# Kernel tuning notes

Hardware: AMD Instinct MI355X
Metric: run time of the kernel (lower is better)

The kernel has to match this reference:

```python
import jax, jax.numpy as jnp
import numpy as np

TRIPLET_MARGIN = 0.2
ATN_ALPHA = 0.1
ATN_BETA = 1.05
ATN_WEIGHT = 1.0
EPS = 1e-8


def _normalize(x):
    return x / jnp.maximum(jnp.linalg.norm(x, axis=-1, keepdims=True), EPS)


def _cos_dist_rowwise(a, b):  # [N,d],[N,d] -> [N]
    return 1.0 - jnp.sum(_normalize(a) * _normalize(b), axis=-1)


def _cos_dist_matrix(a, b):  # [N,d],[C,d] -> [N,C]
    return 1.0 - _normalize(a) @ _normalize(b).T


def setup_inputs() -> dict:
    key = jax.random.key(0)
    ks = jax.random.split(key, 5)
    N, D, C = 65536, 512, 16
    return {
        "anchor": jax.random.normal(ks[0], (N, D), jnp.float32),
        "positive": jax.random.normal(ks[1], (N, D), jnp.float32),
        "negative": jax.random.normal(ks[2], (N, D), jnp.float32),
        "embeddings": jax.random.normal(ks[3], (N, D), jnp.float32),
        "labels": jax.random.randint(ks[4], (N,), 0, C, jnp.int32),
        "num_classes": C,
    }


def reference(anchor, positive, negative, embeddings, labels, num_classes):
    # --- Triplet loss ---
    pos_dist = _cos_dist_rowwise(anchor, positive)
    neg_dist = _cos_dist_rowwise(anchor, negative)
    triplet = jnp.mean(jax.nn.relu(pos_dist - neg_dist + TRIPLET_MARGIN))

    # --- Augmented Triplet (ATN) loss ---
    N = embeddings.shape[0]
    counts = jax.ops.segment_sum(jnp.ones((N,), embeddings.dtype), labels,
                                 num_segments=num_classes)  # [C]
    sums = jax.ops.segment_sum(embeddings, labels, num_segments=num_classes)  # [C,d]
    centroids = sums / jnp.maximum(counts, 1.0)[:, None]
    present = counts > 0  # [C]

    cdist = _cos_dist_matrix(centroids, centroids)  # [C,C]
    eye = jnp.eye(num_classes, dtype=bool)
    pair = (cdist <= ATN_BETA) & ~eye & present[:, None] & present[None, :]  # symmetric
    pair_f = pair.astype(embeddings.dtype)
    cnt = pair_f.sum(axis=1)  # close pairs per class [C]

    D = _cos_dist_matrix(embeddings, centroids)  # [N,C]
    d_own = jnp.take_along_axis(D, labels[:, None], axis=1)[:, 0]  # [N]
    w = cnt[labels]  # multiplicity of each sample in intra/inter terms [N]

    intra_sum = jnp.sum(w * jax.nn.relu(d_own - ATN_ALPHA))
    inter_sum = jnp.sum(pair_f[labels] * jax.nn.relu(ATN_BETA - D))
    n_terms = jnp.sum(w)  # identical count for intra and inter lists
    safe_n = jnp.maximum(n_terms, 1.0)
    atn = jnp.where(n_terms > 0, intra_sum / safe_n + inter_sum / safe_n, 0.0)

    return triplet + ATN_WEIGHT * atn
```

## Files before the change

### kernel.cpp

```cpp
#include <hip/hip_runtime.h>

#define EPSN   1e-8f
#define MARGIN 0.2f
#define ALPHA  0.1f
#define BETA   1.05f
#define DIM    512
#define NCLS   16
#define NSTR   516

typedef __attribute__((ext_vector_type(8))) short short8;
typedef __attribute__((ext_vector_type(4))) float f32x4;
typedef __attribute__((ext_vector_type(4))) float nf4;

__device__ __forceinline__ unsigned short f2bf(float f) {
    unsigned u = __float_as_uint(f);
    return (unsigned short)((u + 0x7FFFu + ((u >> 16) & 1u)) >> 16);
}
__device__ __forceinline__ short8 pack8(float4 x0, float4 x1) {
    short8 r;
    r[0] = (short)f2bf(x0.x); r[1] = (short)f2bf(x0.y);
    r[2] = (short)f2bf(x0.z); r[3] = (short)f2bf(x0.w);
    r[4] = (short)f2bf(x1.x); r[5] = (short)f2bf(x1.y);
    r[6] = (short)f2bf(x1.z); r[7] = (short)f2bf(x1.w);
    return r;
}


__global__ __launch_bounds__(256) void k_init(const int* __restrict__ L,
                                              float* __restrict__ wsw,
                                              int* __restrict__ cpart, int N) {
    __shared__ int hist[NCLS];
    int t = threadIdx.x, bid = blockIdx.x;
    int gid = bid * 256 + t;
    for (int i = gid; i < 8192; i += 64 * 256) wsw[i] = 0.f;
    if (t < NCLS) hist[t] = 0;
    __syncthreads();
    int chunk = N >> 6;
    int base = bid * chunk;
    for (int i = t * 4; i < chunk; i += 1024) {
        int4 l4 = *(const int4*)(L + base + i);
        atomicAdd(&hist[l4.x], 1);
        atomicAdd(&hist[l4.y], 1);
        atomicAdd(&hist[l4.z], 1);
        atomicAdd(&hist[l4.w], 1);
    }
    __syncthreads();
    if (t < NCLS) cpart[bid * NCLS + t] = hist[t];
}

__global__ __launch_bounds__(256) void k_triplet(const float* __restrict__ A,
                                                 const float* __restrict__ P,
                                                 const float* __restrict__ Q,
                                                 float* __restrict__ tripart, int N) {
    __shared__ float red[4];
    int t = threadIdx.x, lane = t & 63, wid = t >> 6;
    int g = lane >> 4, seg = lane & 15;
    int gw = blockIdx.x * 4 + wid, nw = gridDim.x * 4;
    int nquad = N >> 2;
    float tri = 0.f;
    for (int quad = gw; quad < nquad; quad += 2 * nw) {
        int quadB = quad + nw;
        bool hasB = quadB < nquad;
        size_t base0 = (size_t)(quad * 4 + g) * DIM + seg * 4;
        size_t base1 = hasB ? ((size_t)(quadB * 4 + g) * DIM + seg * 4) : base0;
        nf4 a0[8], p0[8], q0[8], a1[8], p1[8], q1[8];
#pragma unroll
        for (int i = 0; i < 8; ++i) a0[i] = __builtin_nontemporal_load((const nf4*)(A + base0 + i * 64));
#pragma unroll
        for (int i = 0; i < 8; ++i) p0[i] = __builtin_nontemporal_load((const nf4*)(P + base0 + i * 64));
#pragma unroll
        for (int i = 0; i < 8; ++i) q0[i] = __builtin_nontemporal_load((const nf4*)(Q + base0 + i * 64));
#pragma unroll
        for (int i = 0; i < 8; ++i) a1[i] = __builtin_nontemporal_load((const nf4*)(A + base1 + i * 64));
#pragma unroll
        for (int i = 0; i < 8; ++i) p1[i] = __builtin_nontemporal_load((const nf4*)(P + base1 + i * 64));
#pragma unroll
        for (int i = 0; i < 8; ++i) q1[i] = __builtin_nontemporal_load((const nf4*)(Q + base1 + i * 64));
        {
            float sa = 0, sp = 0, sn = 0, dap = 0, dan = 0;
#pragma unroll
            for (int i = 0; i < 8; ++i) {
                sa  = fmaf(a0[i].x,a0[i].x, fmaf(a0[i].y,a0[i].y, fmaf(a0[i].z,a0[i].z, fmaf(a0[i].w,a0[i].w, sa))));
                sp  = fmaf(p0[i].x,p0[i].x, fmaf(p0[i].y,p0[i].y, fmaf(p0[i].z,p0[i].z, fmaf(p0[i].w,p0[i].w, sp))));
                sn  = fmaf(q0[i].x,q0[i].x, fmaf(q0[i].y,q0[i].y, fmaf(q0[i].z,q0[i].z, fmaf(q0[i].w,q0[i].w, sn))));
                dap = fmaf(a0[i].x,p0[i].x, fmaf(a0[i].y,p0[i].y, fmaf(a0[i].z,p0[i].z, fmaf(a0[i].w,p0[i].w, dap))));
                dan = fmaf(a0[i].x,q0[i].x, fmaf(a0[i].y,q0[i].y, fmaf(a0[i].z,q0[i].z, fmaf(a0[i].w,q0[i].w, dan))));
            }
#pragma unroll
            for (int o = 1; o < 16; o <<= 1) {
                sa  += __shfl_xor(sa,  o);
                sp  += __shfl_xor(sp,  o);
                sn  += __shfl_xor(sn,  o);
                dap += __shfl_xor(dap, o);
                dan += __shfl_xor(dan, o);
            }
            if (seg == 0) {
                float na = fmaxf(sqrtf(sa), EPSN);
                float np = fmaxf(sqrtf(sp), EPSN);
                float nn = fmaxf(sqrtf(sn), EPSN);
                tri += fmaxf((1.f - dap / (na * np)) - (1.f - dan / (na * nn)) + MARGIN, 0.f);
            }
        }
        if (hasB) {
            float sa = 0, sp = 0, sn = 0, dap = 0, dan = 0;
#pragma unroll
            for (int i = 0; i < 8; ++i) {
                sa  = fmaf(a1[i].x,a1[i].x, fmaf(a1[i].y,a1[i].y, fmaf(a1[i].z,a1[i].z, fmaf(a1[i].w,a1[i].w, sa))));
                sp  = fmaf(p1[i].x,p1[i].x, fmaf(p1[i].y,p1[i].y, fmaf(p1[i].z,p1[i].z, fmaf(p1[i].w,p1[i].w, sp))));
                sn  = fmaf(q1[i].x,q1[i].x, fmaf(q1[i].y,q1[i].y, fmaf(q1[i].z,q1[i].z, fmaf(q1[i].w,q1[i].w, sn))));
                dap = fmaf(a1[i].x,p1[i].x, fmaf(a1[i].y,p1[i].y, fmaf(a1[i].z,p1[i].z, fmaf(a1[i].w,p1[i].w, dap))));
                dan = fmaf(a1[i].x,q1[i].x, fmaf(a1[i].y,q1[i].y, fmaf(a1[i].z,q1[i].z, fmaf(a1[i].w,q1[i].w, dan))));
            }
#pragma unroll
            for (int o = 1; o < 16; o <<= 1) {
                sa  += __shfl_xor(sa,  o);
                sp  += __shfl_xor(sp,  o);
                sn  += __shfl_xor(sn,  o);
                dap += __shfl_xor(dap, o);
                dan += __shfl_xor(dan, o);
            }
            if (seg == 0) {
                float na = fmaxf(sqrtf(sa), EPSN);
                float np = fmaxf(sqrtf(sp), EPSN);
                float nn = fmaxf(sqrtf(sn), EPSN);
                tri += fmaxf((1.f - dap / (na * np)) - (1.f - dan / (na * nn)) + MARGIN, 0.f);
            }
        }
    }
    tri += __shfl_xor(tri, 16);
    tri += __shfl_xor(tri, 32);
    if (lane == 0) red[wid] = tri;
    __syncthreads();
    if (t == 0) tripart[blockIdx.x] = red[0] + red[1] + red[2] + red[3];
}

__global__ __launch_bounds__(256) void k_segsum(const float* __restrict__ E,
                                                const int* __restrict__ L,
                                                float* __restrict__ sums, int N) {
    __shared__ float acc[NCLS * 256];
    int t = threadIdx.x;
    int half = blockIdx.x & 1;
    int rg = blockIdx.x >> 1;
    int rpg = N >> 9;
    int r0 = rg * rpg;
    for (int i = t; i < NCLS * 256; i += 256) acc[i] = 0.f;
    __syncthreads();
    const float* Eh = E + half * 256 + t;
    for (int r = r0; r < r0 + rpg; r += 16) {
        int l[16];
        float v[16];
#pragma unroll
        for (int i = 0; i < 16; ++i) l[i] = L[r + i];
#pragma unroll
        for (int i = 0; i < 16; ++i) v[i] = Eh[(size_t)(r + i) * DIM];
#pragma unroll
        for (int i = 0; i < 16; ++i) acc[l[i] * 256 + t] += v[i];
    }
    __syncthreads();
#pragma unroll
    for (int c = 0; c < NCLS; ++c)
        atomicAdd(&sums[c * DIM + half * 256 + t], acc[c * 256 + t]);
}

__global__ __launch_bounds__(256) void k_centroid(const int* __restrict__ cpart,
                                                  const float* __restrict__ sums,
                                                  unsigned short* __restrict__ ncnh,
                                                  float* __restrict__ pr_g,
                                                  float* __restrict__ cf_g,
                                                  float* __restrict__ ntv) {
    __shared__ float ncns[NCLS * NSTR];
    __shared__ float prs[NCLS * NCLS];
    __shared__ float cntl[NCLS];
    int t = threadIdx.x;
    if (t < NCLS) {
        int s = 0;
        for (int b = 0; b < 64; ++b) s += cpart[b * NCLS + t];
        cntl[t] = (float)s;
    }
    __syncthreads();
    {
        int c = t >> 4, sI = t & 15;
        float inv = 1.f / fmaxf(cntl[c], 1.f);
        float4 v[8];
        float ssq = 0.f;
#pragma unroll
        for (int i = 0; i < 8; ++i) {
            v[i] = *(const float4*)(sums + c * DIM + sI * 32 + i * 4);
            v[i].x *= inv; v[i].y *= inv; v[i].z *= inv; v[i].w *= inv;
            ssq = fmaf(v[i].x, v[i].x, fmaf(v[i].y, v[i].y, fmaf(v[i].z, v[i].z, fmaf(v[i].w, v[i].w, ssq))));
        }
#pragma unroll
        for (int o = 1; o < 16; o <<= 1) ssq += __shfl_xor(ssq, o);
        float rs = 1.f / fmaxf(sqrtf(ssq), EPSN);
#pragma unroll
        for (int i = 0; i < 8; ++i) {
            float4 w = v[i];
            w.x *= rs; w.y *= rs; w.z *= rs; w.w *= rs;
            *(float4*)&ncns[c * NSTR + sI * 32 + i * 4] = w;
            ushort4 h;
            h.x = f2bf(w.x); h.y = f2bf(w.y); h.z = f2bf(w.z); h.w = f2bf(w.w);
            *(ushort4*)(ncnh + c * DIM + sI * 32 + i * 4) = h;
        }
    }
    __syncthreads();
    {
        int i = t >> 4, j = t & 15;
        float dot = 0.f;
        for (int d = 0; d < DIM; d += 4) {
            float4 a = *(const float4*)&ncns[i * NSTR + d];
            float4 b = *(const float4*)&ncns[j * NSTR + d];
            dot = fmaf(a.x, b.x, fmaf(a.y, b.y, fmaf(a.z, b.z, fmaf(a.w, b.w, dot))));
        }
        float cd = 1.f - dot;
        float pf = (cd <= BETA && i != j && cntl[i] > 0.f && cntl[j] > 0.f) ? 1.f : 0.f;
        prs[t] = pf;
        pr_g[t] = pf;
    }
    __syncthreads();
    if (t < NCLS) {
        float s = 0.f;
#pragma unroll
        for (int k = 0; k < NCLS; ++k) s += prs[t * 16 + k];
        cf_g[t] = s;
        cntl[t] = cntl[t] * s;
    }
    __syncthreads();
    if (t == 0) {
        float nt = 0.f;
#pragma unroll
        for (int k = 0; k < NCLS; ++k) nt += cntl[k];
        ntv[0] = nt;
        ntv[1] = 1.f / fmaxf(nt, 1.f);
    }
}

__global__ __launch_bounds__(256) void k_atn(const float* __restrict__ E,
                                             const int* __restrict__ L,
                                             const unsigned short* __restrict__ ncnh,
                                             const float* __restrict__ pr_g,
                                             const float* __restrict__ cf_g,
                                             float* __restrict__ atnpart,
                                             int nblk, int N) {
    __shared__ short bsh[16 * 4 * 16 * 8];
    __shared__ float pr[NCLS * NCLS];
    __shared__ float cf[NCLS];
    __shared__ float red[8];
    int t = threadIdx.x, lane = t & 63, wid = t >> 6;
    pr[t] = pr_g[t];
    if (t < NCLS) cf[t] = cf_g[t];
    {
        int ccol = t & 15, ckg = (t >> 4) & 3, sb = t >> 6;
#pragma unroll
        for (int i = 0; i < 4; ++i) {
            int s = sb * 4 + i;
            uint4 w = *(const uint4*)(ncnh + ccol * DIM + s * 32 + ckg * 8);
            *(uint4*)&bsh[((s * 4 + ckg) * 16 + ccol) * 8] = w;
        }
    }
    __syncthreads();

    int col = lane & 15;
    int kg = lane >> 4;
    const short* bbase = &bsh[(kg * 16 + col) * 8];

    float inter = 0.f, intra = 0.f;
    int gw = blockIdx.x * 4 + wid, nw = gridDim.x * 4;
    int ntile = N >> 4;
    for (int tile = gw; tile < ntile; tile += nw) {
        int rowb = tile << 4;
        int lval = L[rowb + col];
        const float* ar = E + (size_t)(rowb + col) * DIM + kg * 8;
        f32x4 ac0 = {0,0,0,0}, ac1 = {0,0,0,0}, ac2 = {0,0,0,0}, ac3 = {0,0,0,0};
        float ss0 = 0.f, ss1 = 0.f, ss2 = 0.f, ss3 = 0.f;
#pragma unroll
        for (int sg = 0; sg < 4; ++sg) {
            float4 x[8];
#pragma unroll
            for (int k = 0; k < 8; ++k)
                x[k] = *(const float4*)(ar + sg * 128 + (k >> 1) * 32 + (k & 1) * 4);
            {
                float4 u = x[0], v = x[1];
                short8 bf = *(const short8*)(bbase + (sg * 4 + 0) * 512);
                ss0 = fmaf(u.x,u.x, fmaf(u.y,u.y, fmaf(u.z,u.z, fmaf(u.w,u.w, ss0))));
                ss0 = fmaf(v.x,v.x, fmaf(v.y,v.y, fmaf(v.z,v.z, fmaf(v.w,v.w, ss0))));
                ac0 = __builtin_amdgcn_mfma_f32_16x16x32_bf16(pack8(u, v), bf, ac0, 0, 0, 0);
            }
            {
                float4 u = x[2], v = x[3];
                short8 bf = *(const short8*)(bbase + (sg * 4 + 1) * 512);
                ss1 = fmaf(u.x,u.x, fmaf(u.y,u.y, fmaf(u.z,u.z, fmaf(u.w,u.w, ss1))));
                ss1 = fmaf(v.x,v.x, fmaf(v.y,v.y, fmaf(v.z,v.z, fmaf(v.w,v.w, ss1))));
                ac1 = __builtin_amdgcn_mfma_f32_16x16x32_bf16(pack8(u, v), bf, ac1, 0, 0, 0);
            }
            {
                float4 u = x[4], v = x[5];
                short8 bf = *(const short8*)(bbase + (sg * 4 + 2) * 512);
                ss2 = fmaf(u.x,u.x, fmaf(u.y,u.y, fmaf(u.z,u.z, fmaf(u.w,u.w, ss2))));
                ss2 = fmaf(v.x,v.x, fmaf(v.y,v.y, fmaf(v.z,v.z, fmaf(v.w,v.w, ss2))));
                ac2 = __builtin_amdgcn_mfma_f32_16x16x32_bf16(pack8(u, v), bf, ac2, 0, 0, 0);
            }
            {
                float4 u = x[6], v = x[7];
                short8 bf = *(const short8*)(bbase + (sg * 4 + 3) * 512);
                ss3 = fmaf(u.x,u.x, fmaf(u.y,u.y, fmaf(u.z,u.z, fmaf(u.w,u.w, ss3))));
                ss3 = fmaf(v.x,v.x, fmaf(v.y,v.y, fmaf(v.z,v.z, fmaf(v.w,v.w, ss3))));
                ac3 = __builtin_amdgcn_mfma_f32_16x16x32_bf16(pack8(u, v), bf, ac3, 0, 0, 0);
            }
        }
        f32x4 accv = (ac0 + ac1) + (ac2 + ac3);
        float ss = (ss0 + ss1) + (ss2 + ss3);
        ss += __shfl_xor(ss, 16);
        ss += __shfl_xor(ss, 32);
#pragma unroll
        for (int reg = 0; reg < 4; ++reg) {
            int row = kg * 4 + reg;
            float s2 = __shfl(ss, row);
            int lab = __shfl(lval, row);
            float rinv = 1.f / fmaxf(sqrtf(s2), EPSN);
            float d = 1.f - accv[reg] * rinv;
            inter += pr[lab * 16 + col] * fmaxf(BETA - d, 0.f);
            if (col == lab) intra += cf[lab] * fmaxf(d - ALPHA, 0.f);
        }
    }
#pragma unroll
    for (int o = 32; o > 0; o >>= 1) {
        inter += __shfl_xor(inter, o);
        intra += __shfl_xor(intra, o);
    }
    if (lane == 0) { red[wid] = intra; red[4 + wid] = inter; }
    __syncthreads();
    if (t == 0) {
        atnpart[blockIdx.x]        = red[0] + red[1] + red[2] + red[3];
        atnpart[nblk + blockIdx.x] = red[4] + red[5] + red[6] + red[7];
    }
}

__global__ __launch_bounds__(256) void k_final(const float* __restrict__ tripart,
                                               const float* __restrict__ atnpart,
                                               const float* __restrict__ ntv,
                                               float* __restrict__ out,
                                               float invN, int ntri, int natn) {
    __shared__ float r[12];
    int t = threadIdx.x, lane = t & 63, wid = t >> 6;
    float s_tri = 0.f, s_in = 0.f, s_ie = 0.f;
    for (int i = t; i < ntri; i += 256) s_tri += tripart[i];
    for (int i = t; i < natn; i += 256) { s_in += atnpart[i]; s_ie += atnpart[natn + i]; }
#pragma unroll
    for (int o = 1; o < 64; o <<= 1) {
        s_tri += __shfl_xor(s_tri, o);
        s_in  += __shfl_xor(s_in,  o);
        s_ie  += __shfl_xor(s_ie,  o);
    }
    if (lane == 0) { r[wid] = s_tri; r[4 + wid] = s_in; r[8 + wid] = s_ie; }
    __syncthreads();
    if (t == 0) {
        float tri = r[0] + r[1] + r[2] + r[3];
        float in2 = r[4] + r[5] + r[6] + r[7];
        float ie2 = r[8] + r[9] + r[10] + r[11];
        float nt = ntv[0];
        float atnv = (nt > 0.f) ? (in2 + ie2) * ntv[1] : 0.f;
        out[0] = tri * invN + atnv;
    }
}

extern "C" void kernel_launch(void* const* d_in, const int* in_sizes, int n_in,
                              void* d_out, int out_size, void* d_ws, size_t ws_size,
                              hipStream_t stream) {
    const float* A = (const float*)d_in[0];
    const float* P = (const float*)d_in[1];
    const float* Q = (const float*)d_in[2];
    const float* E = (const float*)d_in[3];
    const int*   L = (const int*)d_in[4];
    int N = in_sizes[0] / DIM;

    float*          wsf     = (float*)d_ws;
    float*          sums    = wsf;
    int*            cpart   = (int*)(wsf + 8192);
    unsigned short* ncnh    = (unsigned short*)(wsf + 9216);
    float*          prg     = wsf + 13312;
    float*          cfg     = wsf + 13568;
    float*          ntv     = wsf + 13584;
    float*          tripart = wsf + 13600;
    float*          atnpart = wsf + 15648;

    k_init     <<<64,   256, 0, stream>>>(L, wsf, cpart, N);
    k_triplet  <<<2048, 256, 0, stream>>>(A, P, Q, tripart, N);
    k_segsum   <<<1024, 256, 0, stream>>>(E, L, sums, N);
    k_centroid <<<1,    256, 0, stream>>>(cpart, sums, ncnh, prg, cfg, ntv);
    k_atn      <<<512,  256, 0, stream>>>(E, L, ncnh, prg, cfg, atnpart, 512, N);
    k_final    <<<1,    256, 0, stream>>>(tripart, atnpart, ntv, (float*)d_out,
                                          1.f / (float)N, 2048, 512);
}
```

Before: 140.9 us.

## Fuse triplet and segment-sum kernels into one heterogeneous launch

Merges the triplet-loss kernel and the per-class segment-sum kernel into a single 2048-block launch. Every fourth block does segment-sum work (512 blocks, each covering twice as many rows), and the remaining 1536 blocks do triplet work. The goal is to overlap the two bandwidth-bound streams and remove one launch and its tail. The trade-off is fewer triplet blocks, a larger LDS footprint for every block (the 16 KB accumulator is now shared), and possible load imbalance between the two roles.

```diff
diff --git a/kernel.cpp b/kernel.cpp
--- a/kernel.cpp
+++ b/kernel.cpp
@@ -48,118 +48,122 @@
     if (t < NCLS) cpart[bid * NCLS + t] = hist[t];
 }
 
-__global__ __launch_bounds__(256) void k_triplet(const float* __restrict__ A,
-                                                 const float* __restrict__ P,
-                                                 const float* __restrict__ Q,
-                                                 float* __restrict__ tripart, int N) {
-    __shared__ float red[4];
+__global__ __launch_bounds__(256) void k_fused(const float* __restrict__ A,
+                                               const float* __restrict__ P,
+                                               const float* __restrict__ Q,
+                                               const float* __restrict__ E,
+                                               const int* __restrict__ L,
+                                               float* __restrict__ sums,
+                                               float* __restrict__ tripart, int N) {
+    __shared__ float acc[NCLS * 256];
     int t = threadIdx.x, lane = t & 63, wid = t >> 6;
-    int g = lane >> 4, seg = lane & 15;
-    int gw = blockIdx.x * 4 + wid, nw = gridDim.x * 4;
-    int nquad = N >> 2;
-    float tri = 0.f;
-    for (int quad = gw; quad < nquad; quad += 2 * nw) {
-        int quadB = quad + nw;
-        bool hasB = quadB < nquad;
-        size_t base0 = (size_t)(quad * 4 + g) * DIM + seg * 4;
-        size_t base1 = hasB ? ((size_t)(quadB * 4 + g) * DIM + seg * 4) : base0;
-        nf4 a0[8], p0[8], q0[8], a1[8], p1[8], q1[8];
-#pragma unroll
-        for (int i = 0; i < 8; ++i) a0[i] = __builtin_nontemporal_load((const nf4*)(A + base0 + i * 64));
-#pragma unroll
-        for (int i = 0; i < 8; ++i) p0[i] = __builtin_nontemporal_load((const nf4*)(P + base0 + i * 64));
-#pragma unroll
-        for (int i = 0; i < 8; ++i) q0[i] = __builtin_nontemporal_load((const nf4*)(Q + base0 + i * 64));
-#pragma unroll
-        for (int i = 0; i < 8; ++i) a1[i] = __builtin_nontemporal_load((const nf4*)(A + base1 + i * 64));
-#pragma unroll
-        for (int i = 0; i < 8; ++i) p1[i] = __builtin_nontemporal_load((const nf4*)(P + base1 + i * 64));
-#pragma unroll
-        for (int i = 0; i < 8; ++i) q1[i] = __builtin_nontemporal_load((const nf4*)(Q + base1 + i * 64));
-        {
-            float sa = 0, sp = 0, sn = 0, dap = 0, dan = 0;
-#pragma unroll
-            for (int i = 0; i < 8; ++i) {
-                sa  = fmaf(a0[i].x,a0[i].x, fmaf(a0[i].y,a0[i].y, fmaf(a0[i].z,a0[i].z, fmaf(a0[i].w,a0[i].w, sa))));
-                sp  = fmaf(p0[i].x,p0[i].x, fmaf(p0[i].y,p0[i].y, fmaf(p0[i].z,p0[i].z, fmaf(p0[i].w,p0[i].w, sp))));
-                sn  = fmaf(q0[i].x,q0[i].x, fmaf(q0[i].y,q0[i].y, fmaf(q0[i].z,q0[i].z, fmaf(q0[i].w,q0[i].w, sn))));
-                dap = fmaf(a0[i].x,p0[i].x, fmaf(a0[i].y,p0[i].y, fmaf(a0[i].z,p0[i].z, fmaf(a0[i].w,p0[i].w, dap))));
-                dan = fmaf(a0[i].x,q0[i].x, fmaf(a0[i].y,q0[i].y, fmaf(a0[i].z,q0[i].z, fmaf(a0[i].w,q0[i].w, dan))));
-            }
-#pragma unroll
-            for (int o = 1; o < 16; o <<= 1) {
-                sa  += __shfl_xor(sa,  o);
-                sp  += __shfl_xor(sp,  o);
-                sn  += __shfl_xor(sn,  o);
-                dap += __shfl_xor(dap, o);
-                dan += __shfl_xor(dan, o);
-            }
-            if (seg == 0) {
-                float na = fmaxf(sqrtf(sa), EPSN);
-                float np = fmaxf(sqrtf(sp), EPSN);
-                float nn = fmaxf(sqrtf(sn), EPSN);
-                tri += fmaxf((1.f - dap / (na * np)) - (1.f - dan / (na * nn)) + MARGIN, 0.f);
-            }
-        }
-        if (hasB) {
-            float sa = 0, sp = 0, sn = 0, dap = 0, dan = 0;
-#pragma unroll
-            for (int i = 0; i < 8; ++i) {
-                sa  = fmaf(a1[i].x,a1[i].x, fmaf(a1[i].y,a1[i].y, fmaf(a1[i].z,a1[i].z, fmaf(a1[i].w,a1[i].w, sa))));
-                sp  = fmaf(p1[i].x,p1[i].x, fmaf(p1[i].y,p1[i].y, fmaf(p1[i].z,p1[i].z, fmaf(p1[i].w,p1[i].w, sp))));
-                sn  = fmaf(q1[i].x,q1[i].x, fmaf(q1[i].y,q1[i].y, fmaf(q1[i].z,q1[i].z, fmaf(q1[i].w,q1[i].w, sn))));
-                dap = fmaf(a1[i].x,p1[i].x, fmaf(a1[i].y,p1[i].y, fmaf(a1[i].z,p1[i].z, fmaf(a1[i].w,p1[i].w, dap))));
-                dan = fmaf(a1[i].x,q1[i].x, fmaf(a1[i].y,q1[i].y, fmaf(a1[i].z,q1[i].z, fmaf(a1[i].w,q1[i].w, dan))));
-            }
-#pragma unroll
-            for (int o = 1; o < 16; o <<= 1) {
-                sa  += __shfl_xor(sa,  o);
-                sp  += __shfl_xor(sp,  o);
-                sn  += __shfl_xor(sn,  o);
-                dap += __shfl_xor(dap, o);
-                dan += __shfl_xor(dan, o);
-            }
-            if (seg == 0) {
-                float na = fmaxf(sqrtf(sa), EPSN);
-                float np = fmaxf(sqrtf(sp), EPSN);
-                float nn = fmaxf(sqrtf(sn), EPSN);
-                tri += fmaxf((1.f - dap / (na * np)) - (1.f - dan / (na * nn)) + MARGIN, 0.f);
-            }
-        }
-    }
-    tri += __shfl_xor(tri, 16);
-    tri += __shfl_xor(tri, 32);
-    if (lane == 0) red[wid] = tri;
-    __syncthreads();
-    if (t == 0) tripart[blockIdx.x] = red[0] + red[1] + red[2] + red[3];
-}
-
-__global__ __launch_bounds__(256) void k_segsum(const float* __restrict__ E,
-                                                const int* __restrict__ L,
-                                                float* __restrict__ sums, int N) {
-    __shared__ float acc[NCLS * 256];
-    int t = threadIdx.x;
-    int half = blockIdx.x & 1;
-    int rg = blockIdx.x >> 1;
-    int rpg = N >> 9;
-    int r0 = rg * rpg;
-    for (int i = t; i < NCLS * 256; i += 256) acc[i] = 0.f;
-    __syncthreads();
-    const float* Eh = E + half * 256 + t;
-    for (int r = r0; r < r0 + rpg; r += 16) {
-        int l[16];
-        float v[16];
-#pragma unroll
-        for (int i = 0; i < 16; ++i) l[i] = L[r + i];
-#pragma unroll
-        for (int i = 0; i < 16; ++i) v[i] = Eh[(size_t)(r + i) * DIM];
-#pragma unroll
-        for (int i = 0; i < 16; ++i) acc[l[i] * 256 + t] += v[i];
-    }
-    __syncthreads();
-#pragma unroll
-    for (int c = 0; c < NCLS; ++c)
-        atomicAdd(&sums[c * DIM + half * 256 + t], acc[c * 256 + t]);
+    int bid = blockIdx.x;
+
+    if ((bid & 3) == 3) {
+        int sb = bid >> 2;
+        int half = sb & 1;
+        int rg = sb >> 1;
+        int rpg = N >> 8;
+        int r0 = rg * rpg;
+        for (int i = t; i < NCLS * 256; i += 256) acc[i] = 0.f;
+        __syncthreads();
+        const float* Eh = E + half * 256 + t;
+        for (int r = r0; r < r0 + rpg; r += 16) {
+            int l[16];
+            float v[16];
+#pragma unroll
+            for (int i = 0; i < 16; ++i) l[i] = L[r + i];
+#pragma unroll
+            for (int i = 0; i < 16; ++i) v[i] = Eh[(size_t)(r + i) * DIM];
+#pragma unroll
+            for (int i = 0; i < 16; ++i) acc[l[i] * 256 + t] += v[i];
+        }
+        __syncthreads();
+#pragma unroll
+        for (int c = 0; c < NCLS; ++c)
+            atomicAdd(&sums[c * DIM + half * 256 + t], acc[c * 256 + t]);
+    } else {
+        int trank = bid - (bid >> 2);
+        const int NW = 1536 * 4;
+        int g = lane >> 4, seg = lane & 15;
+        int gw = trank * 4 + wid;
+        int nquad = N >> 2;
+        float tri = 0.f;
+        for (int quad = gw; quad < nquad; quad += 2 * NW) {
+            int quadB = quad + NW;
+            bool hasB = quadB < nquad;
+            size_t base0 = (size_t)(quad * 4 + g) * DIM + seg * 4;
+            size_t base1 = hasB ? ((size_t)(quadB * 4 + g) * DIM + seg * 4) : base0;
+            nf4 a0[8], p0[8], q0[8], a1[8], p1[8], q1[8];
+#pragma unroll
+            for (int i = 0; i < 8; ++i) a0[i] = __builtin_nontemporal_load((const nf4*)(A + base0 + i * 64));
+#pragma unroll
+            for (int i = 0; i < 8; ++i) p0[i] = __builtin_nontemporal_load((const nf4*)(P + base0 + i * 64));
+#pragma unroll
+            for (int i = 0; i < 8; ++i) q0[i] = __builtin_nontemporal_load((const nf4*)(Q + base0 + i * 64));
+#pragma unroll
+            for (int i = 0; i < 8; ++i) a1[i] = __builtin_nontemporal_load((const nf4*)(A + base1 + i * 64));
+#pragma unroll
+            for (int i = 0; i < 8; ++i) p1[i] = __builtin_nontemporal_load((const nf4*)(P + base1 + i * 64));
+#pragma unroll
+            for (int i = 0; i < 8; ++i) q1[i] = __builtin_nontemporal_load((const nf4*)(Q + base1 + i * 64));
+            {
+                float sa = 0, sp = 0, sn = 0, dap = 0, dan = 0;
+#pragma unroll
+                for (int i = 0; i < 8; ++i) {
+                    sa  = fmaf(a0[i].x,a0[i].x, fmaf(a0[i].y,a0[i].y, fmaf(a0[i].z,a0[i].z, fmaf(a0[i].w,a0[i].w, sa))));
+                    sp  = fmaf(p0[i].x,p0[i].x, fmaf(p0[i].y,p0[i].y, fmaf(p0[i].z,p0[i].z, fmaf(p0[i].w,p0[i].w, sp))));
+                    sn  = fmaf(q0[i].x,q0[i].x, fmaf(q0[i].y,q0[i].y, fmaf(q0[i].z,q0[i].z, fmaf(q0[i].w,q0[i].w, sn))));
+                    dap = fmaf(a0[i].x,p0[i].x, fmaf(a0[i].y,p0[i].y, fmaf(a0[i].z,p0[i].z, fmaf(a0[i].w,p0[i].w, dap))));
+                    dan = fmaf(a0[i].x,q0[i].x, fmaf(a0[i].y,q0[i].y, fmaf(a0[i].z,q0[i].z, fmaf(a0[i].w,q0[i].w, dan))));
+                }
+#pragma unroll
+                for (int o = 1; o < 16; o <<= 1) {
+                    sa  += __shfl_xor(sa,  o);
+                    sp  += __shfl_xor(sp,  o);
+                    sn  += __shfl_xor(sn,  o);
+                    dap += __shfl_xor(dap, o);
+                    dan += __shfl_xor(dan, o);
+                }
+                if (seg == 0) {
+                    float na = fmaxf(sqrtf(sa), EPSN);
+                    float np = fmaxf(sqrtf(sp), EPSN);
+                    float nn = fmaxf(sqrtf(sn), EPSN);
+                    tri += fmaxf((1.f - dap / (na * np)) - (1.f - dan / (na * nn)) + MARGIN, 0.f);
+                }
+            }
+            if (hasB) {
+                float sa = 0, sp = 0, sn = 0, dap = 0, dan = 0;
+#pragma unroll
+                for (int i = 0; i < 8; ++i) {
+                    sa  = fmaf(a1[i].x,a1[i].x, fmaf(a1[i].y,a1[i].y, fmaf(a1[i].z,a1[i].z, fmaf(a1[i].w,a1[i].w, sa))));
+                    sp  = fmaf(p1[i].x,p1[i].x, fmaf(p1[i].y,p1[i].y, fmaf(p1[i].z,p1[i].z, fmaf(p1[i].w,p1[i].w, sp))));
+                    sn  = fmaf(q1[i].x,q1[i].x, fmaf(q1[i].y,q1[i].y, fmaf(q1[i].z,q1[i].z, fmaf(q1[i].w,q1[i].w, sn))));
+                    dap = fmaf(a1[i].x,p1[i].x, fmaf(a1[i].y,p1[i].y, fmaf(a1[i].z,p1[i].z, fmaf(a1[i].w,p1[i].w, dap))));
+                    dan = fmaf(a1[i].x,q1[i].x, fmaf(a1[i].y,q1[i].y, fmaf(a1[i].z,q1[i].z, fmaf(a1[i].w,q1[i].w, dan))));
+                }
+#pragma unroll
+                for (int o = 1; o < 16; o <<= 1) {
+                    sa  += __shfl_xor(sa,  o);
+                    sp  += __shfl_xor(sp,  o);
+                    sn  += __shfl_xor(sn,  o);
+                    dap += __shfl_xor(dap, o);
+                    dan += __shfl_xor(dan, o);
+                }
+                if (seg == 0) {
+                    float na = fmaxf(sqrtf(sa), EPSN);
+                    float np = fmaxf(sqrtf(sp), EPSN);
+                    float nn = fmaxf(sqrtf(sn), EPSN);
+                    tri += fmaxf((1.f - dap / (na * np)) - (1.f - dan / (na * nn)) + MARGIN, 0.f);
+                }
+            }
+        }
+        tri += __shfl_xor(tri, 16);
+        tri += __shfl_xor(tri, 32);
+        if (lane == 0) acc[wid] = tri;
+        __syncthreads();
+        if (t == 0) tripart[trank] = acc[0] + acc[1] + acc[2] + acc[3];
+    }
 }
 
 __global__ __launch_bounds__(256) void k_centroid(const int* __restrict__ cpart,
@@ -384,10 +388,9 @@
     float*          atnpart = wsf + 15648;
 
     k_init     <<<64,   256, 0, stream>>>(L, wsf, cpart, N);
-    k_triplet  <<<2048, 256, 0, stream>>>(A, P, Q, tripart, N);
-    k_segsum   <<<1024, 256, 0, stream>>>(E, L, sums, N);
+    k_fused    <<<2048, 256, 0, stream>>>(A, P, Q, E, L, sums, tripart, N);
     k_centroid <<<1,    256, 0, stream>>>(cpart, sums, ncnh, prg, cfg, ntv);
     k_atn      <<<512,  256, 0, stream>>>(E, L, ncnh, prg, cfg, atnpart, 512, N);
     k_final    <<<1,    256, 0, stream>>>(tripart, atnpart, ntv, (float*)d_out,
-                                          1.f / (float)N, 2048, 512);
-}
+                                          1.f / (float)N, 1536, 512);
+}
```

Result: no change. 140.2 us (-0.5%).
